# Kernel tuning notes

Measured on AMD Instinct MI355X. Metric: run time of the kernel, lower is better.

## Reference

```python
import jax, jax.numpy as jnp
import numpy as np

B, H, W, C = 32, 64, 64, 256
WS, SS = 8, 4            # window_size, shift_size
HEADS, HD = C // 32, 32  # heads, head_dim
SCALE = HD ** -0.5
WS2 = WS * WS
NW = (H // WS) * (W // WS)  # windows per image


def _rel_pos_indices(ws):
    # matches ShiftedWindowAttention.get_indices
    x = np.arange(ws)
    y1, x1, y2, x2 = np.meshgrid(x, x, x, x, indexing='ij')
    idx = (y1 - y2 + ws - 1) * (2 * ws - 1) + (x1 - x2 + ws - 1)
    return jnp.asarray(idx.reshape(-1), dtype=jnp.int32)  # (ws^4,)


def _shift_mask(h, w, ws, ss):
    # standard Swin shifted-window mask: True where attention is forbidden
    img = np.zeros((h, w), np.int32)
    cnt = 0
    for hs in (slice(0, -ws), slice(-ws, -ss), slice(-ss, None)):
        for wsl in (slice(0, -ws), slice(-ws, -ss), slice(-ss, None)):
            img[hs, wsl] = cnt
            cnt += 1
    win = img.reshape(h // ws, ws, w // ws, ws).transpose(0, 2, 1, 3).reshape(-1, ws * ws)
    return jnp.asarray(win[:, :, None] != win[:, None, :])  # (nW, ws^2, ws^2)


REL_IDX = _rel_pos_indices(WS)
MASK = _shift_mask(H, W, WS, SS)


def setup_inputs() -> dict:
    key = jax.random.key(0)
    ks = jax.random.split(key, 6)
    s = C ** -0.5
    return {
        'x': jax.random.normal(ks[0], (B, H * W, C), jnp.float32),
        'w_qkv': jax.random.normal(ks[1], (C, 3 * C), jnp.float32) * s,
        'b_qkv': jnp.zeros((3 * C,), jnp.float32),
        'w_out': jax.random.normal(ks[2], (C, C), jnp.float32) * s,
        'b_out': jnp.zeros((C,), jnp.float32),
        'pos_enc': jax.random.normal(ks[3], (HEADS, (2 * WS - 1) ** 2), jnp.float32) * 0.02,
    }


def reference(x, w_qkv, b_qkv, w_out, b_out, pos_enc):
    b = x.shape[0]
    xi = x.reshape(b, H, W, C)
    xi = jnp.roll(xi, (-SS, -SS), axis=(1, 2))  # cyclic shift
    nh, nw = H // WS, W // WS
    # window partition -> (b*nW, ws^2, C)
    xw = xi.reshape(b, nh, WS, nw, WS, C).transpose(0, 1, 3, 2, 4, 5).reshape(b * NW, WS2, C)
    qkv = xw @ w_qkv + b_qkv
    q, k, v = jnp.split(qkv, 3, axis=-1)
    split = lambda t: t.reshape(b * NW, WS2, HEADS, HD).transpose(0, 2, 1, 3)
    q, k, v = split(q), split(k), split(v)  # (b*nW, heads, ws^2, hd)
    attn = jnp.einsum('whqd,whkd->whqk', q, k) * SCALE
    bias = pos_enc[:, REL_IDX].reshape(HEADS, WS2, WS2)
    attn = attn + bias[None]
    # shifted-window mask per window position
    attn = attn.reshape(b, NW, HEADS, WS2, WS2)
    attn = jnp.where(MASK[None, :, None], -jnp.inf, attn)
    attn = jax.nn.softmax(attn.reshape(b * NW, HEADS, WS2, WS2), axis=-1)
    out = jnp.einsum('whqk,whkd->whqd', attn, v)
    out = out.transpose(0, 2, 1, 3).reshape(b * NW, WS2, C)
    out = out @ w_out + b_out
    # reverse window partition
    out = out.reshape(b, nh, nw, WS, WS, C).transpose(0, 1, 3, 2, 4, 5).reshape(b, H, W, C)
    out = jnp.roll(out, (SS, SS), axis=(1, 2))  # reverse cyclic shift
    return out.reshape(b, H * W, C)
```

## Files before the change

### kernel.cpp

```cpp
#include <hip/hip_runtime.h>

typedef __bf16 bf16_t;
typedef __bf16 bf16x4 __attribute__((ext_vector_type(4)));
typedef __bf16 bf16x8 __attribute__((ext_vector_type(8)));
typedef float f32x4 __attribute__((ext_vector_type(4)));

#define SCALE_LOG2E 0.25510803519787995f
#define LOG2E 1.4426950408889634f
#define SWZ(row) (((row) & 15) << 4)

__device__ __forceinline__ f32x4 mk4(float4 v) { return (f32x4){v.x, v.y, v.z, v.w}; }
__device__ __forceinline__ bf16x8 pack2(f32x4 a, f32x4 b) {
  bf16x4 lo = __builtin_convertvector(a, bf16x4);
  bf16x4 hi = __builtin_convertvector(b, bf16x4);
  return __builtin_shufflevector(lo, hi, 0, 1, 2, 3, 4, 5, 6, 7);
}

__global__ __launch_bounds__(256, 1) void prep_weights(
    const float* __restrict__ wqkv, const float* __restrict__ wout,
    bf16_t* __restrict__ wqkvT, bf16_t* __restrict__ woutT) {
  int i = blockIdx.x * 256 + threadIdx.x;
  int n = i >> 8, k = i & 255;
  if (n < 768) {
    int s = n >> 8, hl = n & 255;
    int src;
    if (s < 2) {
      int h = hl >> 5, w = hl & 31, c = (w >> 4) & 1, r = w & 15;
      src = 32 * h + 8 * (r >> 2) + 4 * c + (r & 3);
    } else {
      src = hl;
    }
    float v = wqkv[k * 768 + s * 256 + src];
    if (s == 0) v *= SCALE_LOG2E;
    wqkvT[n * 256 + k] = (bf16_t)v;
  } else {
    int m = n - 768;
    woutT[m * 256 + k] = (bf16_t)wout[k * 256 + m];
  }
}

__global__ __launch_bounds__(256, 1) void prep_bias(
    const float* __restrict__ pos_enc, bf16_t* __restrict__ biasI) {
  int i = blockIdx.x * 256 + threadIdx.x;
  int ii = i & 3, lane = (i >> 2) & 63, nt = (i >> 8) & 3, qt = (i >> 10) & 3, h = i >> 12;
  int g = lane >> 4, cc = lane & 15;
  int q = 32 * (qt >> 1) + 4 * (qt & 1) + 8 * (cc >> 2) + (cc & 3);
  int key = 32 * (nt >> 1) + 4 * (nt & 1) + 8 * g + ii;
  int qy = q >> 3, qx = q & 7, ky = key >> 3, kx = key & 7;
  biasI[i] = (bf16_t)(pos_enc[h * 225 + (qy - ky + 7) * 15 + (qx - kx + 7)] * LOG2E);
}

__global__ __launch_bounds__(256, 2) void swin_attn(
    const float* __restrict__ x,
    const float* __restrict__ b_qkv,
    const float* __restrict__ b_out,
    const bf16_t* __restrict__ wqkvT,
    const bf16_t* __restrict__ woutT,
    const bf16_t* __restrict__ biasI,
    float* __restrict__ out) {
  __shared__ __attribute__((aligned(16))) char smem[65536];
  char* Osm = smem + 32768;

  const int tid  = threadIdx.x;
  const int wid  = blockIdx.x;
  const int bb   = wid >> 6;
  const int w64  = wid & 63;
  const int wy   = w64 >> 3, wx = w64 & 7;
  const int wave = tid >> 6, lane = tid & 63;
  const int g    = lane >> 4, cc = lane & 15;
  const bool maskY = (wy == 7), maskX = (wx == 7);
  const int rb = 8 * (cc >> 2) + (cc & 3);

  {
    const float* xb = x + (size_t)bb * 4096 * 256;
    #pragma unroll
    for (int it = 0; it < 16; ++it) {
      int fi = tid + 256 * it;
      int r = fi >> 6, c4 = fi & 63;
      int hh = (8 * wy + (r >> 3) + 4) & 63;
      int ww = (8 * wx + (r & 7) + 4) & 63;
      const float4 v = ((const float4*)(xb + ((size_t)hh * 64 + ww) * 256))[c4];
      bf16x4 pk = __builtin_convertvector(mk4(v), bf16x4);
      *(bf16x4*)(smem + r * 512 + ((8 * c4) ^ SWZ(r))) = pk;
    }
  }
  __syncthreads();

  #pragma unroll
  for (int hh = 0; hh < 2; ++hh) {
    const int h = 2 * wave + hh;

    f32x4 aq[2][4], ak[2][4], av[4][2];
    #pragma unroll
    for (int c = 0; c < 2; ++c)
      #pragma unroll
      for (int t = 0; t < 4; ++t) {
        aq[c][t] = (f32x4){0.f, 0.f, 0.f, 0.f};
        ak[c][t] = (f32x4){0.f, 0.f, 0.f, 0.f};
        av[t][c] = (f32x4){0.f, 0.f, 0.f, 0.f};
      }
    const bf16_t* wq = wqkvT + (size_t)(      32 * h) * 256;
    const bf16_t* wk = wqkvT + (size_t)(256 + 32 * h) * 256;
    const bf16_t* wv = wqkvT + (size_t)(512 + 32 * h) * 256;
    #pragma unroll
    for (int ks = 0; ks < 8; ++ks) {
      bf16x8 aks[4];
      #pragma unroll
      for (int t = 0; t < 4; ++t) {
        int row = 32 * (t >> 1) + 4 * (t & 1) + rb;
        aks[t] = *(const bf16x8*)(smem + row * 512 + ((64 * ks + 16 * g) ^ SWZ(row)));
      }
      #pragma unroll
      for (int c = 0; c < 2; ++c) {
        int ro = (16 * c + cc) * 256 + 32 * ks + 8 * g;
        bf16x8 fq = *(const bf16x8*)&wq[ro];
        bf16x8 fk = *(const bf16x8*)&wk[ro];
        bf16x8 fv = *(const bf16x8*)&wv[ro];
        #pragma unroll
        for (int t = 0; t < 4; ++t) {
          aq[c][t] = __builtin_amdgcn_mfma_f32_16x16x32_bf16(fq, aks[t], aq[c][t], 0, 0, 0);
          ak[c][t] = __builtin_amdgcn_mfma_f32_16x16x32_bf16(fk, aks[t], ak[c][t], 0, 0, 0);
          av[t][c] = __builtin_amdgcn_mfma_f32_16x16x32_bf16(aks[t], fv, av[t][c], 0, 0, 0);
        }
      }
    }

    bf16x8 qp[4], kp[4], vp[2][2];
    {
      f32x4 bq0 = mk4(*(const float4*)&b_qkv[32 * h + 8 * g]) * SCALE_LOG2E;
      f32x4 bq1 = mk4(*(const float4*)&b_qkv[32 * h + 8 * g + 4]) * SCALE_LOG2E;
      f32x4 bk0 = mk4(*(const float4*)&b_qkv[256 + 32 * h + 8 * g]);
      f32x4 bk1 = mk4(*(const float4*)&b_qkv[256 + 32 * h + 8 * g + 4]);
      #pragma unroll
      for (int t = 0; t < 4; ++t) {
        qp[t] = pack2(aq[0][t] + bq0, aq[1][t] + bq1);
        kp[t] = pack2(ak[0][t] + bk0, ak[1][t] + bk1);
      }
      #pragma unroll
      for (int c = 0; c < 2; ++c) {
        float bv = b_qkv[512 + 32 * h + 16 * c + cc];
        f32x4 bv4 = (f32x4){bv, bv, bv, bv};
        #pragma unroll
        for (int ks = 0; ks < 2; ++ks)
          vp[c][ks] = pack2(av[2 * ks][c] + bv4, av[2 * ks + 1][c] + bv4);
      }
    }

    f32x4 sacc[4][4];
    #pragma unroll
    for (int nt = 0; nt < 4; ++nt)
      #pragma unroll
      for (int qt = 0; qt < 4; ++qt) sacc[nt][qt] = (f32x4){0.f, 0.f, 0.f, 0.f};
    #pragma unroll
    for (int qt = 0; qt < 4; ++qt)
      #pragma unroll
      for (int nt = 0; nt < 4; ++nt)
        sacc[nt][qt] = __builtin_amdgcn_mfma_f32_16x16x32_bf16(kp[nt], qp[qt], sacc[nt][qt], 0, 0, 0);

    bf16x8 pf[4][2];
    const bf16_t* bI = biasI + h * 4096 + lane * 4;
    #pragma unroll
    for (int qt = 0; qt < 4; ++qt) {
      f32x4 sv[4];
      #pragma unroll
      for (int nt = 0; nt < 4; ++nt) {
        bool dead = (maskY && ((qt < 2) != (nt < 2))) || (maskX && ((qt & 1) != (nt & 1)));
        if (dead) {
          sv[nt] = (f32x4){-3.0e38f, -3.0e38f, -3.0e38f, -3.0e38f};
        } else {
          bf16x4 bb = *(const bf16x4*)&bI[(qt * 4 + nt) * 256];
          sv[nt] = sacc[nt][qt] + __builtin_convertvector(bb, f32x4);
        }
      }
      float mx = -3.0e38f;
      #pragma unroll
      for (int nt = 0; nt < 4; ++nt)
        #pragma unroll
        for (int i = 0; i < 4; ++i) mx = fmaxf(mx, sv[nt][i]);
      mx = fmaxf(mx, __shfl_xor(mx, 16));
      mx = fmaxf(mx, __shfl_xor(mx, 32));
      float sum = 0.f;
      #pragma unroll
      for (int nt = 0; nt < 4; ++nt)
        #pragma unroll
        for (int i = 0; i < 4; ++i) {
          float e = exp2f(sv[nt][i] - mx);
          sv[nt][i] = e;
          sum += e;
        }
      sum += __shfl_xor(sum, 16);
      sum += __shfl_xor(sum, 32);
      float rinv = 1.0f / sum;
      #pragma unroll
      for (int nt = 0; nt < 4; ++nt) sv[nt] *= rinv;
      pf[qt][0] = pack2(sv[0], sv[1]);
      pf[qt][1] = pack2(sv[2], sv[3]);
    }

    f32x4 oacc[2][4];
    #pragma unroll
    for (int c = 0; c < 2; ++c)
      #pragma unroll
      for (int qt = 0; qt < 4; ++qt) oacc[c][qt] = (f32x4){0.f, 0.f, 0.f, 0.f};
    #pragma unroll
    for (int ks = 0; ks < 2; ++ks)
      #pragma unroll
      for (int c = 0; c < 2; ++c)
        #pragma unroll
        for (int qt = 0; qt < 4; ++qt)
          oacc[c][qt] = __builtin_amdgcn_mfma_f32_16x16x32_bf16(vp[c][ks], pf[qt][ks], oacc[c][qt], 0, 0, 0);

    #pragma unroll
    for (int c = 0; c < 2; ++c)
      #pragma unroll
      for (int qt = 0; qt < 4; ++qt) {
        int tok = 32 * (qt >> 1) + 4 * (qt & 1) + rb;
        bf16x4 ob = __builtin_convertvector(oacc[c][qt], bf16x4);
        *(bf16x4*)(Osm + tok * 512 +
                   ((2 * (64 * wave + 32 * hh + 16 * c + 4 * g)) ^ SWZ(tok))) = ob;
      }
  }
  __syncthreads();

  {
    f32x4 pacc[4][4];
    #pragma unroll
    for (int c = 0; c < 4; ++c)
      #pragma unroll
      for (int t = 0; t < 4; ++t) pacc[c][t] = (f32x4){0.f, 0.f, 0.f, 0.f};
    #pragma unroll
    for (int ks = 0; ks < 8; ++ks) {
      bf16x8 of[4];
      #pragma unroll
      for (int t = 0; t < 4; ++t) {
        int row = 16 * t + cc;
        of[t] = *(const bf16x8*)(Osm + row * 512 + ((64 * ks + 16 * g) ^ SWZ(row)));
      }
      #pragma unroll
      for (int c2 = 0; c2 < 4; ++c2) {
        bf16x8 wf = *(const bf16x8*)&woutT[(size_t)(64 * wave + 16 * c2 + cc) * 256 + 32 * ks + 8 * g];
        #pragma unroll
        for (int t = 0; t < 4; ++t)
          pacc[c2][t] = __builtin_amdgcn_mfma_f32_16x16x32_bf16(wf, of[t], pacc[c2][t], 0, 0, 0);
      }
    }
    #pragma unroll
    for (int c2 = 0; c2 < 4; ++c2) {
      int ch = 64 * wave + 16 * c2 + 4 * g;
      float4 bo4 = *(const float4*)&b_out[ch];
      #pragma unroll
      for (int t = 0; t < 4; ++t) {
        int q = 16 * t + cc;
        int hh2 = (8 * wy + (q >> 3) + 4) & 63;
        int ww2 = (8 * wx + (q & 7) + 4) & 63;
        float4 st;
        st.x = pacc[c2][t][0] + bo4.x;
        st.y = pacc[c2][t][1] + bo4.y;
        st.z = pacc[c2][t][2] + bo4.z;
        st.w = pacc[c2][t][3] + bo4.w;
        *(float4*)&out[(((size_t)bb * 4096) + hh2 * 64 + ww2) * 256 + ch] = st;
      }
    }
  }
}

extern "C" void kernel_launch(void* const* d_in, const int* in_sizes, int n_in,
                              void* d_out, int out_size, void* d_ws, size_t ws_size,
                              hipStream_t stream) {
  const float* x       = (const float*)d_in[0];
  const float* w_qkv   = (const float*)d_in[1];
  const float* b_qkv   = (const float*)d_in[2];
  const float* w_out   = (const float*)d_in[3];
  const float* b_out   = (const float*)d_in[4];
  const float* pos_enc = (const float*)d_in[5];
  float* out = (float*)d_out;

  bf16_t* wqkvT = (bf16_t*)d_ws;
  bf16_t* woutT = wqkvT + 768 * 256;
  bf16_t* biasI = woutT + 256 * 256;

  prep_weights<<<dim3(1024), dim3(256), 0, stream>>>(w_qkv, w_out, wqkvT, woutT);
  prep_bias<<<dim3(128), dim3(256), 0, stream>>>(pos_enc, biasI);
  swin_attn<<<dim3(2048), dim3(256), 0, stream>>>(
      x, b_qkv, b_out, wqkvT, woutT, biasI, out);
}
```

Measured before the change: 188.7 us.

## Use one wave per head with 512-thread blocks and shared LDS buffer

New measurement: 431.8 us. +128.8%, slower.

```diff
diff --git a/kernel.cpp b/kernel.cpp
--- a/kernel.cpp
+++ b/kernel.cpp
@@ -50,7 +50,7 @@
   biasI[i] = (bf16_t)(pos_enc[h * 225 + (qy - ky + 7) * 15 + (qx - kx + 7)] * LOG2E);
 }
 
-__global__ __launch_bounds__(256, 2) void swin_attn(
+__global__ __launch_bounds__(512, 4) void swin_attn(
     const float* __restrict__ x,
     const float* __restrict__ b_qkv,
     const float* __restrict__ b_out,
@@ -58,15 +58,15 @@
     const bf16_t* __restrict__ woutT,
     const bf16_t* __restrict__ biasI,
     float* __restrict__ out) {
-  __shared__ __attribute__((aligned(16))) char smem[65536];
-  char* Osm = smem + 32768;
+  __shared__ __attribute__((aligned(16))) char smem[32768];
 
   const int tid  = threadIdx.x;
   const int wid  = blockIdx.x;
   const int bb   = wid >> 6;
   const int w64  = wid & 63;
   const int wy   = w64 >> 3, wx = w64 & 7;
-  const int wave = tid >> 6, lane = tid & 63;
+  const int h    = tid >> 6;
+  const int lane = tid & 63;
   const int g    = lane >> 4, cc = lane & 15;
   const bool maskY = (wy == 7), maskX = (wx == 7);
   const int rb = 8 * (cc >> 2) + (cc & 3);
@@ -74,8 +74,8 @@
   {
     const float* xb = x + (size_t)bb * 4096 * 256;
     #pragma unroll
-    for (int it = 0; it < 16; ++it) {
-      int fi = tid + 256 * it;
+    for (int it = 0; it < 8; ++it) {
+      int fi = tid + 512 * it;
       int r = fi >> 6, c4 = fi & 63;
       int hh = (8 * wy + (r >> 3) + 4) & 63;
       int ww = (8 * wx + (r & 7) + 4) & 63;
@@ -86,22 +86,18 @@
   }
   __syncthreads();
 
-  #pragma unroll
-  for (int hh = 0; hh < 2; ++hh) {
-    const int h = 2 * wave + hh;
-
-    f32x4 aq[2][4], ak[2][4], av[4][2];
+  bf16x8 qp[4], kp[4], vp[2][2];
+  {
+    f32x4 aq[2][4], ak[2][4];
     #pragma unroll
     for (int c = 0; c < 2; ++c)
       #pragma unroll
       for (int t = 0; t < 4; ++t) {
         aq[c][t] = (f32x4){0.f, 0.f, 0.f, 0.f};
         ak[c][t] = (f32x4){0.f, 0.f, 0.f, 0.f};
-        av[t][c] = (f32x4){0.f, 0.f, 0.f, 0.f};
-      }
-    const bf16_t* wq = wqkvT + (size_t)(      32 * h) * 256;
+      }
+    const bf16_t* wq = wqkvT + (size_t)(32 * h) * 256;
     const bf16_t* wk = wqkvT + (size_t)(256 + 32 * h) * 256;
-    const bf16_t* wv = wqkvT + (size_t)(512 + 32 * h) * 256;
     #pragma unroll
     for (int ks = 0; ks < 8; ++ks) {
       bf16x8 aks[4];
@@ -115,37 +111,58 @@
         int ro = (16 * c + cc) * 256 + 32 * ks + 8 * g;
         bf16x8 fq = *(const bf16x8*)&wq[ro];
         bf16x8 fk = *(const bf16x8*)&wk[ro];
-        bf16x8 fv = *(const bf16x8*)&wv[ro];
         #pragma unroll
         for (int t = 0; t < 4; ++t) {
           aq[c][t] = __builtin_amdgcn_mfma_f32_16x16x32_bf16(fq, aks[t], aq[c][t], 0, 0, 0);
           ak[c][t] = __builtin_amdgcn_mfma_f32_16x16x32_bf16(fk, aks[t], ak[c][t], 0, 0, 0);
+        }
+      }
+    }
+    f32x4 bq0 = mk4(*(const float4*)&b_qkv[32 * h + 8 * g]) * SCALE_LOG2E;
+    f32x4 bq1 = mk4(*(const float4*)&b_qkv[32 * h + 8 * g + 4]) * SCALE_LOG2E;
+    f32x4 bk0 = mk4(*(const float4*)&b_qkv[256 + 32 * h + 8 * g]);
+    f32x4 bk1 = mk4(*(const float4*)&b_qkv[256 + 32 * h + 8 * g + 4]);
+    #pragma unroll
+    for (int t = 0; t < 4; ++t) {
+      qp[t] = pack2(aq[0][t] + bq0, aq[1][t] + bq1);
+      kp[t] = pack2(ak[0][t] + bk0, ak[1][t] + bk1);
+    }
+  }
+  {
+    f32x4 av[4][2];
+    #pragma unroll
+    for (int t = 0; t < 4; ++t)
+      #pragma unroll
+      for (int c = 0; c < 2; ++c) av[t][c] = (f32x4){0.f, 0.f, 0.f, 0.f};
+    const bf16_t* wv = wqkvT + (size_t)(512 + 32 * h) * 256;
+    #pragma unroll
+    for (int ks = 0; ks < 8; ++ks) {
+      bf16x8 aks[4];
+      #pragma unroll
+      for (int t = 0; t < 4; ++t) {
+        int row = 32 * (t >> 1) + 4 * (t & 1) + rb;
+        aks[t] = *(const bf16x8*)(smem + row * 512 + ((64 * ks + 16 * g) ^ SWZ(row)));
+      }
+      #pragma unroll
+      for (int c = 0; c < 2; ++c) {
+        bf16x8 fv = *(const bf16x8*)&wv[(16 * c + cc) * 256 + 32 * ks + 8 * g];
+        #pragma unroll
+        for (int t = 0; t < 4; ++t)
           av[t][c] = __builtin_amdgcn_mfma_f32_16x16x32_bf16(aks[t], fv, av[t][c], 0, 0, 0);
-        }
-      }
-    }
-
-    bf16x8 qp[4], kp[4], vp[2][2];
-    {
-      f32x4 bq0 = mk4(*(const float4*)&b_qkv[32 * h + 8 * g]) * SCALE_LOG2E;
-      f32x4 bq1 = mk4(*(const float4*)&b_qkv[32 * h + 8 * g + 4]) * SCALE_LOG2E;
-      f32x4 bk0 = mk4(*(const float4*)&b_qkv[256 + 32 * h + 8 * g]);
-      f32x4 bk1 = mk4(*(const float4*)&b_qkv[256 + 32 * h + 8 * g + 4]);
-      #pragma unroll
-      for (int t = 0; t < 4; ++t) {
-        qp[t] = pack2(aq[0][t] + bq0, aq[1][t] + bq1);
-        kp[t] = pack2(ak[0][t] + bk0, ak[1][t] + bk1);
-      }
-      #pragma unroll
-      for (int c = 0; c < 2; ++c) {
-        float bv = b_qkv[512 + 32 * h + 16 * c + cc];
-        f32x4 bv4 = (f32x4){bv, bv, bv, bv};
-        #pragma unroll
-        for (int ks = 0; ks < 2; ++ks)
-          vp[c][ks] = pack2(av[2 * ks][c] + bv4, av[2 * ks + 1][c] + bv4);
-      }
-    }
-
+      }
+    }
+    #pragma unroll
+    for (int c = 0; c < 2; ++c) {
+      float bv = b_qkv[512 + 32 * h + 16 * c + cc];
+      f32x4 bv4 = (f32x4){bv, bv, bv, bv};
+      #pragma unroll
+      for (int ks = 0; ks < 2; ++ks)
+        vp[c][ks] = pack2(av[2 * ks][c] + bv4, av[2 * ks + 1][c] + bv4);
+    }
+  }
+  __syncthreads();
+
+  {
     f32x4 sacc[4][4];
     #pragma unroll
     for (int nt = 0; nt < 4; ++nt)
@@ -168,8 +185,8 @@
         if (dead) {
           sv[nt] = (f32x4){-3.0e38f, -3.0e38f, -3.0e38f, -3.0e38f};
         } else {
-          bf16x4 bb = *(const bf16x4*)&bI[(qt * 4 + nt) * 256];
-          sv[nt] = sacc[nt][qt] + __builtin_convertvector(bb, f32x4);
+          bf16x4 bb4 = *(const bf16x4*)&bI[(qt * 4 + nt) * 256];
+          sv[nt] = sacc[nt][qt] + __builtin_convertvector(bb4, f32x4);
         }
       }
       float mx = -3.0e38f;
@@ -216,16 +233,15 @@
       for (int qt = 0; qt < 4; ++qt) {
         int tok = 32 * (qt >> 1) + 4 * (qt & 1) + rb;
         bf16x4 ob = __builtin_convertvector(oacc[c][qt], bf16x4);
-        *(bf16x4*)(Osm + tok * 512 +
-                   ((2 * (64 * wave + 32 * hh + 16 * c + 4 * g)) ^ SWZ(tok))) = ob;
+        *(bf16x4*)(smem + tok * 512 + ((2 * (32 * h + 16 * c + 4 * g)) ^ SWZ(tok))) = ob;
       }
   }
   __syncthreads();
 
   {
-    f32x4 pacc[4][4];
-    #pragma unroll
-    for (int c = 0; c < 4; ++c)
+    f32x4 pacc[2][4];
+    #pragma unroll
+    for (int c = 0; c < 2; ++c)
       #pragma unroll
       for (int t = 0; t < 4; ++t) pacc[c][t] = (f32x4){0.f, 0.f, 0.f, 0.f};
     #pragma unroll
@@ -234,19 +250,19 @@
       #pragma unroll
       for (int t = 0; t < 4; ++t) {
         int row = 16 * t + cc;
-        of[t] = *(const bf16x8*)(Osm + row * 512 + ((64 * ks + 16 * g) ^ SWZ(row)));
-      }
-      #pragma unroll
-      for (int c2 = 0; c2 < 4; ++c2) {
-        bf16x8 wf = *(const bf16x8*)&woutT[(size_t)(64 * wave + 16 * c2 + cc) * 256 + 32 * ks + 8 * g];
+        of[t] = *(const bf16x8*)(smem + row * 512 + ((64 * ks + 16 * g) ^ SWZ(row)));
+      }
+      #pragma unroll
+      for (int c2 = 0; c2 < 2; ++c2) {
+        bf16x8 wf = *(const bf16x8*)&woutT[(size_t)(32 * h + 16 * c2 + cc) * 256 + 32 * ks + 8 * g];
         #pragma unroll
         for (int t = 0; t < 4; ++t)
           pacc[c2][t] = __builtin_amdgcn_mfma_f32_16x16x32_bf16(wf, of[t], pacc[c2][t], 0, 0, 0);
       }
     }
     #pragma unroll
-    for (int c2 = 0; c2 < 4; ++c2) {
-      int ch = 64 * wave + 16 * c2 + 4 * g;
+    for (int c2 = 0; c2 < 2; ++c2) {
+      int ch = 32 * h + 16 * c2 + 4 * g;
       float4 bo4 = *(const float4*)&b_out[ch];
       #pragma unroll
       for (int t = 0; t < 4; ++t) {
@@ -281,6 +297,6 @@
 
   prep_weights<<<dim3(1024), dim3(256), 0, stream>>>(w_qkv, w_out, wqkvT, woutT);
   prep_bias<<<dim3(128), dim3(256), 0, stream>>>(pos_enc, biasI);
-  swin_attn<<<dim3(2048), dim3(256), 0, stream>>>(
+  swin_attn<<<dim3(2048), dim3(512), 0, stream>>>(
       x, b_qkv, b_out, wqkvT, woutT, biasI, out);
 }
```
